# Kernel tuning notes

Hardware: AMD Instinct MI355X
Metric: run time of the kernel (lower is better)

The kernel has to match this reference:

```python
import jax, jax.numpy as jnp
import numpy as np

B, W, N, F_IN = 2, 8, 10000, 5
E = 80000
H = 128


def setup_inputs() -> dict:
    key = jax.random.key(0)
    ks = jax.random.split(key, 16)
    s = 0.05
    inp = {
        "x": jax.random.normal(ks[0], (B, W, N, F_IN), dtype=jnp.float32),
        "edge_index": jax.random.randint(ks[1], (2, E), 0, N, dtype=jnp.int64),
        # GCN layer 1 (in_features -> hidden) and layer 2 (hidden -> hidden)
        "gcn1_w": jax.random.normal(ks[2], (F_IN, H), dtype=jnp.float32) * s,
        "gcn1_b": jnp.zeros((H,), dtype=jnp.float32),
        "gcn2_w": jax.random.normal(ks[3], (H, H), dtype=jnp.float32) * s,
        "gcn2_b": jnp.zeros((H,), dtype=jnp.float32),
        # LSTM (torch gate order: i, f, g, o)
        "lstm_w_ih": jax.random.normal(ks[4], (4 * H, H), dtype=jnp.float32) * s,
        "lstm_w_hh": jax.random.normal(ks[5], (4 * H, H), dtype=jnp.float32) * s,
        "lstm_b_ih": jnp.zeros((4 * H,), dtype=jnp.float32),
        "lstm_b_hh": jnp.zeros((4 * H,), dtype=jnp.float32),
        # Decoder MLP: H -> H//2 -> 1
        "dec_w1": jax.random.normal(ks[6], (H, H // 2), dtype=jnp.float32) * s,
        "dec_b1": jnp.zeros((H // 2,), dtype=jnp.float32),
        "dec_w2": jax.random.normal(ks[7], (H // 2, 1), dtype=jnp.float32) * s,
        "dec_b2": jnp.zeros((1,), dtype=jnp.float32),
    }
    return inp


def _forward(x, edge_index, gcn1_w, gcn1_b, gcn2_w, gcn2_b,
             lstm_w_ih, lstm_w_hh, lstm_b_ih, lstm_b_hh,
             dec_w1, dec_b1, dec_w2, dec_b2):
    b, w, n, f_in = x.shape
    h_dim = gcn1_w.shape[1]
    # --- GCN normalization (PyG GCNConv default: add self-loops, sym-norm) ---
    loop = jnp.arange(n, dtype=edge_index.dtype)
    src = jnp.concatenate([edge_index[0], loop])
    dst = jnp.concatenate([edge_index[1], loop])
    deg = jnp.zeros((n,), x.dtype).at[dst].add(jnp.float32(1.0))
    dinv = jax.lax.rsqrt(deg)
    norm = dinv[src] * dinv[dst]  # (E+N,)

    def gcn(h, wm, bias):
        # h: (BW, N, Fin) -> (BW, N, H). Transform-then-aggregate (linear op).
        ht = h @ wm                                   # (BW, N, H)
        msg = ht[:, src, :] * norm[None, :, None]      # (BW, E+N, H)
        agg = jnp.zeros_like(ht).at[:, dst, :].add(msg)
        return agg + bias

    xf = x.reshape(b * w, n, f_in)
    h = jax.nn.relu(gcn(xf, gcn1_w, gcn1_b))   # dropout is identity at eval
    h = jax.nn.relu(gcn(h, gcn2_w, gcn2_b))

    # (BW, N, H) -> (B, N, W, H) -> (B*N, W, H): per-node temporal sequences
    h = h.reshape(b, w, n, h_dim).transpose(0, 2, 1, 3).reshape(b * n, w, h_dim)

    # --- single-layer LSTM, keep only last hidden state ---
    def step(carry, xt):
        hp, cp = carry
        gates = xt @ lstm_w_ih.T + hp @ lstm_w_hh.T + lstm_b_ih + lstm_b_hh
        i, f, g, o = jnp.split(gates, 4, axis=-1)
        c = jax.nn.sigmoid(f) * cp + jax.nn.sigmoid(i) * jnp.tanh(g)
        hn = jax.nn.sigmoid(o) * jnp.tanh(c)
        return (hn, c), None

    init = (jnp.zeros((b * n, h_dim), x.dtype), jnp.zeros((b * n, h_dim), x.dtype))
    (h_last, _), _ = jax.lax.scan(step, init, h.transpose(1, 0, 2))  # scan over W

    # --- MLP decoder ---
    d = jax.nn.relu(h_last @ dec_w1 + dec_b1)
    pred = (d @ dec_w2 + dec_b2)[..., 0]
    return pred.reshape(b, n)


def reference(x, edge_index, gcn1_w, gcn1_b, gcn2_w, gcn2_b,
              lstm_w_ih, lstm_w_hh, lstm_b_ih, lstm_b_hh,
              dec_w1, dec_b1, dec_w2, dec_b2):
    return _forward(x, edge_index, gcn1_w, gcn1_b, gcn2_w, gcn2_b,
                    lstm_w_ih, lstm_w_hh, lstm_b_ih, lstm_b_hh,
                    dec_w1, dec_b1, dec_w2, dec_b2)
```

## Files before the change

### kernel.cpp

```cpp
#include <hip/hip_runtime.h>
#include <hip/hip_fp16.h>
#include <cstdint>
#include <cstddef>

#define Bn   2
#define Wn   8
#define Nn   10000
#define Fin  5
#define En   80000
#define Hn   128
#define BWn  (Bn*Wn)
#define ROWS (BWn*Nn)
#define MR   (Bn*Nn)
#define LROWS 32

typedef _Float16 half8 __attribute__((ext_vector_type(8)));
typedef float f32x4 __attribute__((ext_vector_type(4)));

#define LOG2E 1.44269504088896f

__device__ __forceinline__ float fast_sigmoid(float x) {
    return __builtin_amdgcn_rcpf(1.f + __builtin_amdgcn_exp2f(-LOG2E * x));
}
__device__ __forceinline__ float fast_tanh(float x) {
    return fmaf(-2.f, __builtin_amdgcn_rcpf(1.f + __builtin_amdgcn_exp2f(2.f * LOG2E * x)), 1.f);
}

__global__ __launch_bounds__(256) void setup_kernel(
    const int* __restrict__ ei, const float* __restrict__ bih, const float* __restrict__ bhh,
    const float* __restrict__ wih, const float* __restrict__ whh,
    const float* __restrict__ g2w, const float* __restrict__ x,
    int* __restrict__ counts, float* __restrict__ bsum,
    _Float16* __restrict__ wif, _Float16* __restrict__ whf,
    _Float16* __restrict__ g2wt, float* __restrict__ xt) {
    __shared__ float buf[6400];
    const int b = blockIdx.x;
    const int tid = threadIdx.x;
    if (b < 313) {
        int e = b * 256 + tid;
        if (e < En) atomicAdd(&counts[ei[En + e]], 1);
    } else if (b < 315) {
        int i = (b - 313) * 256 + tid;
        if (i < 4 * Hn) bsum[i] = bih[i] + bhh[i];
    } else if (b < 891) {
        int i = (b - 315) * 256 + tid;
        if (i < 131072) {
            int idx = i & 65535;
            int j = idx & 7, lane = (idx >> 3) & 63, kt = (idx >> 9) & 3, ct = idx >> 11;
            int n = ct * 16 + (lane & 15);
            int k = kt * 32 + (lane >> 4) * 8 + j;
            if (i < 65536) wif[idx] = (_Float16)wih[n * 128 + k];
            else           whf[idx] = (_Float16)whh[n * 128 + k];
        } else {
            int j = i - 131072;
            int n = j >> 7, k = j & 127;
            g2wt[j] = (_Float16)g2w[k * Hn + n];
        }
    } else {
        const int n0 = (b - 891) * 80;
        for (int i = tid; i < 6400; i += 256) {
            int s = i / 400, r = i - s * 400;
            int node = r / 5, f = r - node * 5;
            buf[(node * 16 + s) * 5 + f] = x[((size_t)s * Nn + n0) * 5 + r];
        }
        __syncthreads();
        float* dst = xt + (size_t)n0 * 80;
        for (int i = tid; i < 6400; i += 256) dst[i] = buf[i];
    }
}

enum { CHUNK = 10 };
static_assert(CHUNK * 1024 >= Nn, "scan chunk");

__global__ __launch_bounds__(1024) void scan_kernel(
    const int* __restrict__ counts, int* __restrict__ row_ptr,
    int* __restrict__ fill_ptr, float* __restrict__ dinv) {
    __shared__ int sums[1024];
    const int t = threadIdx.x;
    const int base = t * CHUNK;
    int cnt[CHUNK];
    int s = 0;
    #pragma unroll
    for (int i = 0; i < CHUNK; ++i) {
        int idx = base + i;
        int v = (idx < Nn) ? counts[idx] + 1 : 0;
        cnt[i] = v; s += v;
    }
    sums[t] = s;
    __syncthreads();
    for (int off = 1; off < 1024; off <<= 1) {
        int v = (t >= off) ? sums[t - off] : 0;
        __syncthreads();
        sums[t] += v;
        __syncthreads();
    }
    int excl = (t == 0) ? 0 : sums[t - 1];
    #pragma unroll
    for (int i = 0; i < CHUNK; ++i) {
        int idx = base + i;
        if (idx < Nn) {
            row_ptr[idx] = excl;
            fill_ptr[idx] = excl;
            dinv[idx] = rsqrtf((float)cnt[i]);
            excl += cnt[i];
        }
    }
    if (t == 1023) row_ptr[Nn] = excl;
}

__global__ void fill_kernel(const int* __restrict__ ei,
                            const float* __restrict__ dinv,
                            int* fill_ptr, int* __restrict__ col,
                            float* __restrict__ wgt) {
    int i = blockIdx.x * blockDim.x + threadIdx.x;
    if (i < Nn) {
        int p = atomicAdd(&fill_ptr[i], 1);
        col[p] = i;
        wgt[p] = dinv[i] * dinv[i];
    } else if (i < Nn + En) {
        int e = i - Nn;
        int s = ei[e];
        int d = ei[En + e];
        int p = atomicAdd(&fill_ptr[d], 1);
        col[p] = s;
        wgt[p] = dinv[s] * dinv[d];
    }
}

__global__ __launch_bounds__(128) void agg_x_kernel(
    const float* __restrict__ xt, const int* __restrict__ row_ptr,
    const int* __restrict__ col, const float* __restrict__ wgt,
    float* __restrict__ aggx) {
    const int n = blockIdx.x;
    const int t = threadIdx.x;
    const int s = t >> 3, f = t & 7;
    if (f >= Fin) return;
    const int start = row_ptr[n], end = row_ptr[n + 1];
    const int off = s * 5 + f;
    float acc = 0.f;
    for (int e = start; e < end; ++e)
        acc = fmaf(wgt[e], xt[(size_t)col[e] * 80 + off], acc);
    aggx[(size_t)n * 80 + off] = acc;
}

__global__ __launch_bounds__(256) void gcn2_fused_kernel(
    const float* __restrict__ aggx, const float* __restrict__ w1,
    const float* __restrict__ b1, const _Float16* __restrict__ g2wt,
    _Float16* __restrict__ C) {
    __shared__ __align__(16) _Float16 s_buf[128][136];
    __shared__ _Float16 Bs[128][40];
    const int tid = threadIdx.x;
    const int m0 = blockIdx.x * 128;
    {
        const int rg = tid >> 4;
        const int cg = tid & 15;
        float wreg[Fin][8], breg[8];
        #pragma unroll
        for (int k = 0; k < 8; ++k) breg[k] = b1[cg * 8 + k];
        #pragma unroll
        for (int f = 0; f < Fin; ++f)
            #pragma unroll
            for (int k = 0; k < 8; ++k) wreg[f][k] = w1[f * Hn + cg * 8 + k];
        #pragma unroll
        for (int rr = 0; rr < 8; ++rr) {
            const float* ar = aggx + (size_t)(m0 + rg * 8 + rr) * Fin;
            float a[Fin];
            #pragma unroll
            for (int f = 0; f < Fin; ++f) a[f] = ar[f];
            half8 v;
            #pragma unroll
            for (int k = 0; k < 8; ++k) {
                float s = breg[k];
                #pragma unroll
                for (int f = 0; f < Fin; ++f) s = fmaf(a[f], wreg[f][k], s);
                v[k] = (_Float16)fmaxf(s, 0.f);
            }
            *(half8*)&s_buf[rg * 8 + rr][cg * 8] = v;
        }
    }
    __syncthreads();
    const int wave = tid >> 6, lane = tid & 63;
    const int l = lane & 15, q = lane >> 4;
    const int wm = (wave & 1) * 64, wn = (wave >> 1) * 64;
    f32x4 acc[4][4];
    #pragma unroll
    for (int i = 0; i < 4; ++i)
        #pragma unroll
        for (int j = 0; j < 4; ++j) acc[i][j] = (f32x4){0.f, 0.f, 0.f, 0.f};
    for (int kt = 0; kt < 128; kt += 32) {
        #pragma unroll
        for (int j = 0; j < 2; ++j) {
            int idx = tid + j * 256;
            int r = idx >> 2, c = (idx & 3) * 8;
            *(half8*)&Bs[r][c] = *(const half8*)(g2wt + (size_t)r * 128 + kt + c);
        }
        __syncthreads();
        half8 af[4], bf[4];
        #pragma unroll
        for (int i = 0; i < 4; ++i) af[i] = *(const half8*)&s_buf[wm + i * 16 + l][kt + q * 8];
        #pragma unroll
        for (int j = 0; j < 4; ++j) bf[j] = *(const half8*)&Bs[wn + j * 16 + l][q * 8];
        #pragma unroll
        for (int i = 0; i < 4; ++i)
            #pragma unroll
            for (int j = 0; j < 4; ++j)
                acc[i][j] = __builtin_amdgcn_mfma_f32_16x16x32_f16(
                    af[i], bf[j], acc[i][j], 0, 0, 0);
        __syncthreads();
    }
    #pragma unroll
    for (int j = 0; j < 4; ++j) {
        int ccol = wn + j * 16 + l;
        #pragma unroll
        for (int i = 0; i < 4; ++i)
            #pragma unroll
            for (int r = 0; r < 4; ++r)
                s_buf[wm + i * 16 + q * 4 + r][ccol] = (_Float16)acc[i][j][r];
    }
    __syncthreads();
    const size_t base = (size_t)m0 * 128;
    #pragma unroll
    for (int it = 0; it < 8; ++it) {
        int idx = it * 256 + tid;
        int row = idx >> 4, ch = (idx & 15) * 8;
        *(half8*)(C + base + (size_t)row * 128 + ch) = *(const half8*)&s_buf[row][ch];
    }
}

__global__ __launch_bounds__(256) void gcn_agg2_kernel(
    const _Float16* __restrict__ ht, const int* __restrict__ row_ptr,
    const int* __restrict__ col, const float* __restrict__ wgt,
    const float* __restrict__ bias, _Float16* __restrict__ out) {
    const int n = blockIdx.x;
    const int t = threadIdx.x;
    const int s = t >> 4;
    const int g = (t & 15) * 8;
    const int start = row_ptr[n], end = row_ptr[n + 1];
    float acc[8];
    #pragma unroll
    for (int j = 0; j < 8; ++j) acc[j] = 0.f;
    for (int e = start; e < end; ++e) {
        const int c = col[e];
        const float w = wgt[e];
        half8 v = *(const half8*)(ht + ((size_t)c * BWn + s) * Hn + g);
        #pragma unroll
        for (int j = 0; j < 8; ++j) acc[j] = fmaf(w, (float)v[j], acc[j]);
    }
    half8 o;
    #pragma unroll
    for (int j = 0; j < 8; ++j) o[j] = (_Float16)fmaxf(acc[j] + bias[g + j], 0.f);
    *(half8*)(out + ((size_t)n * BWn + s) * Hn + g) = o;
}

__global__ __launch_bounds__(512, 1) void lstm_fused3_kernel(
    const _Float16* __restrict__ h2, const _Float16* __restrict__ wif,
    const _Float16* __restrict__ whf, const float* __restrict__ bsum,
    const float* __restrict__ dw1, const float* __restrict__ db1,
    const float* __restrict__ dw2, const float* __restrict__ db2,
    float* __restrict__ out) {
    __shared__ __align__(16) _Float16 x_lds[2][LROWS][144];
    __shared__ __align__(16) _Float16 h_lds[2][LROWS][144];
    const int tid = threadIdx.x;
    const int nw = tid >> 6, lane = tid & 63;
    const int l = lane & 15, q = lane >> 4;
    const int r0 = blockIdx.x * LROWS;
    const int srow = tid >> 4, sch = (tid & 15) * 8;
    const int sgrow = r0 + srow;
    const int sb = (sgrow >= Nn) ? 1 : 0;
    const int sn = sgrow - sb * Nn;
    const _Float16* xbase = h2 + ((size_t)sn * BWn + sb * Wn) * 128 + sch;

    half8 wic[4][4], whc[4][4];
    #pragma unroll
    for (int g = 0; g < 4; ++g) {
        int ct = g * 8 + nw;
        #pragma unroll
        for (int kt = 0; kt < 4; ++kt) {
            wic[g][kt] = *(const half8*)(wif + (((size_t)ct * 4 + kt) * 64 + lane) * 8);
            whc[g][kt] = *(const half8*)(whf + (((size_t)ct * 4 + kt) * 64 + lane) * 8);
        }
    }
    float bias[4];
    #pragma unroll
    for (int g = 0; g < 4; ++g) bias[g] = bsum[g * 128 + nw * 16 + l];
    float c_reg[2][4];
    #pragma unroll
    for (int i = 0; i < 2; ++i)
        #pragma unroll
        for (int r = 0; r < 4; ++r) c_reg[i][r] = 0.f;

    *(half8*)&x_lds[0][srow][sch] = *(const half8*)(xbase);
    __syncthreads();

    for (int t = 0; t < Wn; ++t) {
        half8 xv = {0, 0, 0, 0, 0, 0, 0, 0};
        if (t + 1 < Wn) xv = *(const half8*)(xbase + (size_t)(t + 1) * 128);

        f32x4 acc[2][4];
        #pragma unroll
        for (int i = 0; i < 2; ++i)
            #pragma unroll
            for (int g = 0; g < 4; ++g)
                acc[i][g] = (f32x4){bias[g], bias[g], bias[g], bias[g]};

        #pragma unroll
        for (int kt = 0; kt < 4; ++kt) {
            half8 af[2];
            #pragma unroll
            for (int i = 0; i < 2; ++i)
                af[i] = *(const half8*)&x_lds[t & 1][i * 16 + l][kt * 32 + q * 8];
            #pragma unroll
            for (int i = 0; i < 2; ++i)
                #pragma unroll
                for (int g = 0; g < 4; ++g)
                    acc[i][g] = __builtin_amdgcn_mfma_f32_16x16x32_f16(
                        af[i], wic[g][kt], acc[i][g], 0, 0, 0);
        }
        if (t > 0) {
            #pragma unroll
            for (int kt = 0; kt < 4; ++kt) {
                half8 af[2];
                #pragma unroll
                for (int i = 0; i < 2; ++i)
                    af[i] = *(const half8*)&h_lds[t & 1][i * 16 + l][kt * 32 + q * 8];
                #pragma unroll
                for (int i = 0; i < 2; ++i)
                    #pragma unroll
                    for (int g = 0; g < 4; ++g)
                        acc[i][g] = __builtin_amdgcn_mfma_f32_16x16x32_f16(
                            af[i], whc[g][kt], acc[i][g], 0, 0, 0);
            }
        }
        #pragma unroll
        for (int i = 0; i < 2; ++i) {
            #pragma unroll
            for (int r = 0; r < 4; ++r) {
                float si = fast_sigmoid(acc[i][0][r]);
                float sf = fast_sigmoid(acc[i][1][r]);
                float tg = fast_tanh(acc[i][2][r]);
                float so = fast_sigmoid(acc[i][3][r]);
                float cn = sf * c_reg[i][r] + si * tg;
                c_reg[i][r] = cn;
                h_lds[(t + 1) & 1][i * 16 + q * 4 + r][nw * 16 + l] =
                    (_Float16)(so * fast_tanh(cn));
            }
        }
        if (t + 1 < Wn) *(half8*)&x_lds[(t + 1) & 1][srow][sch] = xv;
        __syncthreads();
    }

    #pragma unroll
    for (int rr = 0; rr < 4; ++rr) {
        const int row = nw + rr * 8;
        float d = db1[lane];
        #pragma unroll
        for (int k8 = 0; k8 < 16; ++k8) {
            half8 hv = *(const half8*)&h_lds[0][row][k8 * 8];
            #pragma unroll
            for (int j = 0; j < 8; ++j)
                d = fmaf((float)hv[j], dw1[(k8 * 8 + j) * 64 + lane], d);
        }
        d = fmaxf(d, 0.f);
        float p = d * dw2[lane];
        #pragma unroll
        for (int off = 32; off; off >>= 1) p += __shfl_down(p, off);
        if (lane == 0) out[r0 + row] = p + db2[0];
    }
}


extern "C" void kernel_launch(void* const* d_in, const int* in_sizes, int n_in,
                              void* d_out, int out_size, void* d_ws, size_t ws_size,
                              hipStream_t stream) {
    const float* x   = (const float*)d_in[0];
    const int*   ei  = (const int*)d_in[1];
    const float* g1w = (const float*)d_in[2];
    const float* g1b = (const float*)d_in[3];
    const float* g2w = (const float*)d_in[4];
    const float* g2b = (const float*)d_in[5];
    const float* wih = (const float*)d_in[6];
    const float* whh = (const float*)d_in[7];
    const float* bih = (const float*)d_in[8];
    const float* bhh = (const float*)d_in[9];
    const float* dw1 = (const float*)d_in[10];
    const float* db1 = (const float*)d_in[11];
    const float* dw2 = (const float*)d_in[12];
    const float* db2 = (const float*)d_in[13];
    float* out = (float*)d_out;

    char* p = (char*)d_ws;
    auto alloc = [&](size_t bytes) {
        char* r = p;
        p += (bytes + 255) & ~(size_t)255;
        return r;
    };
    int*      counts   = (int*)     alloc(Nn * 4);
    int*      row_ptr  = (int*)     alloc((Nn + 1) * 4);
    int*      fill_ptr = (int*)     alloc((Nn + 1) * 4);
    float*    dinv     = (float*)   alloc(Nn * 4);
    float*    bsum     = (float*)   alloc(4 * Hn * 4);
    int*      col      = (int*)     alloc((En + Nn) * 4);
    float*    wgt      = (float*)   alloc((En + Nn) * 4);
    _Float16* wif      = (_Float16*)alloc(512 * 128 * 2);
    _Float16* whf      = (_Float16*)alloc(512 * 128 * 2);
    _Float16* g2wt     = (_Float16*)alloc(128 * 128 * 2);
    float*    xt       = (float*)   alloc((size_t)Nn * 80 * 4);
    float*    aggx     = (float*)   alloc((size_t)ROWS * Fin * 4);
    _Float16* htf      = (_Float16*)alloc((size_t)ROWS * Hn * 2);
    _Float16* h2f      = (_Float16*)alloc((size_t)ROWS * Hn * 2);

    hipMemsetAsync(counts, 0, Nn * 4, stream);

    setup_kernel<<<1016, 256, 0, stream>>>(ei, bih, bhh, wih, whh, g2w, x,
                                           counts, bsum, wif, whf, g2wt, xt);
    scan_kernel<<<1, 1024, 0, stream>>>(counts, row_ptr, fill_ptr, dinv);
    fill_kernel<<<(Nn + En + 255) / 256, 256, 0, stream>>>(ei, dinv, fill_ptr, col, wgt);

    agg_x_kernel<<<Nn, 128, 0, stream>>>(xt, row_ptr, col, wgt, aggx);

    gcn2_fused_kernel<<<ROWS / 128, 256, 0, stream>>>(aggx, g1w, g1b, g2wt, htf);

    gcn_agg2_kernel<<<Nn, 256, 0, stream>>>(htf, row_ptr, col, wgt, g2b, h2f);

    lstm_fused3_kernel<<<MR / LROWS, 512, 0, stream>>>(
        h2f, wif, whf, bsum, dw1, db1, dw2, db2, out);
}
```

Baseline: 291.3 us.

## Split decoder out of LSTM kernel and single-buffer the hidden state

Moves the MLP decoder out of the fused LSTM kernel into its own launch. The LSTM now writes its final hidden states to a global fp16 buffer, which the decoder reads back. The hidden-state LDS buffer goes from double to single buffering, which needs an extra barrier per timestep before the hidden state is overwritten. This looks like an unfusion that trades an extra launch and a global round trip, plus more synchronisation, for lower LDS use and simpler LSTM code.

```diff
diff --git a/kernel.cpp b/kernel.cpp
--- a/kernel.cpp
+++ b/kernel.cpp
@@ -252,14 +252,12 @@
     *(half8*)(out + ((size_t)n * BWn + s) * Hn + g) = o;
 }
 
-__global__ __launch_bounds__(512, 1) void lstm_fused3_kernel(
+__global__ __launch_bounds__(512, 1) void lstm_fused2_kernel(
     const _Float16* __restrict__ h2, const _Float16* __restrict__ wif,
     const _Float16* __restrict__ whf, const float* __restrict__ bsum,
-    const float* __restrict__ dw1, const float* __restrict__ db1,
-    const float* __restrict__ dw2, const float* __restrict__ db2,
-    float* __restrict__ out) {
+    _Float16* __restrict__ hf) {
     __shared__ __align__(16) _Float16 x_lds[2][LROWS][144];
-    __shared__ __align__(16) _Float16 h_lds[2][LROWS][144];
+    __shared__ __align__(16) _Float16 h_lds[LROWS][144];
     const int tid = threadIdx.x;
     const int nw = tid >> 6, lane = tid & 63;
     const int l = lane & 15, q = lane >> 4;
@@ -322,7 +320,7 @@
                 half8 af[2];
                 #pragma unroll
                 for (int i = 0; i < 2; ++i)
-                    af[i] = *(const half8*)&h_lds[t & 1][i * 16 + l][kt * 32 + q * 8];
+                    af[i] = *(const half8*)&h_lds[i * 16 + l][kt * 32 + q * 8];
                 #pragma unroll
                 for (int i = 0; i < 2; ++i)
                     #pragma unroll
@@ -331,6 +329,8 @@
                             af[i], whc[g][kt], acc[i][g], 0, 0, 0);
             }
         }
+        __syncthreads();
+
         #pragma unroll
         for (int i = 0; i < 2; ++i) {
             #pragma unroll
@@ -341,31 +341,32 @@
                 float so = fast_sigmoid(acc[i][3][r]);
                 float cn = sf * c_reg[i][r] + si * tg;
                 c_reg[i][r] = cn;
-                h_lds[(t + 1) & 1][i * 16 + q * 4 + r][nw * 16 + l] =
-                    (_Float16)(so * fast_tanh(cn));
+                h_lds[i * 16 + q * 4 + r][nw * 16 + l] = (_Float16)(so * fast_tanh(cn));
             }
         }
         if (t + 1 < Wn) *(half8*)&x_lds[(t + 1) & 1][srow][sch] = xv;
         __syncthreads();
     }
-
-    #pragma unroll
-    for (int rr = 0; rr < 4; ++rr) {
-        const int row = nw + rr * 8;
-        float d = db1[lane];
-        #pragma unroll
-        for (int k8 = 0; k8 < 16; ++k8) {
-            half8 hv = *(const half8*)&h_lds[0][row][k8 * 8];
-            #pragma unroll
-            for (int j = 0; j < 8; ++j)
-                d = fmaf((float)hv[j], dw1[(k8 * 8 + j) * 64 + lane], d);
-        }
-        d = fmaxf(d, 0.f);
-        float p = d * dw2[lane];
-        #pragma unroll
-        for (int off = 32; off; off >>= 1) p += __shfl_down(p, off);
-        if (lane == 0) out[r0 + row] = p + db2[0];
-    }
+    *(half8*)(hf + (size_t)sgrow * 128 + sch) = *(const half8*)&h_lds[srow][sch];
+}
+
+__global__ __launch_bounds__(256) void decoder_kernel(
+    const _Float16* __restrict__ h, const float* __restrict__ w1,
+    const float* __restrict__ b1, const float* __restrict__ w2,
+    const float* __restrict__ b2, float* __restrict__ out) {
+    const int wave = threadIdx.x >> 6;
+    const int lane = threadIdx.x & 63;
+    const int row = blockIdx.x * 4 + wave;
+    if (row >= MR) return;
+    const _Float16* hr = h + (size_t)row * Hn;
+    float d = b1[lane];
+    #pragma unroll 8
+    for (int k = 0; k < Hn; ++k) d = fmaf((float)hr[k], w1[k * 64 + lane], d);
+    d = fmaxf(d, 0.f);
+    float p = d * w2[lane];
+    #pragma unroll
+    for (int off = 32; off; off >>= 1) p += __shfl_down(p, off);
+    if (lane == 0) out[row] = p + b2[0];
 }
 
 
@@ -408,6 +409,7 @@
     float*    aggx     = (float*)   alloc((size_t)ROWS * Fin * 4);
     _Float16* htf      = (_Float16*)alloc((size_t)ROWS * Hn * 2);
     _Float16* h2f      = (_Float16*)alloc((size_t)ROWS * Hn * 2);
+    _Float16* hf       = (_Float16*)alloc((size_t)MR * Hn * 2);
 
     hipMemsetAsync(counts, 0, Nn * 4, stream);
 
@@ -422,6 +424,7 @@
 
     gcn_agg2_kernel<<<Nn, 256, 0, stream>>>(htf, row_ptr, col, wgt, g2b, h2f);
 
-    lstm_fused3_kernel<<<MR / LROWS, 512, 0, stream>>>(
-        h2f, wif, whf, bsum, dw1, db1, dw2, db2, out);
-}
+    lstm_fused2_kernel<<<MR / LROWS, 512, 0, stream>>>(h2f, wif, whf, bsum, hf);
+
+    decoder_kernel<<<(MR + 3) / 4, 256, 0, stream>>>(hf, dw1, db1, dw2, db2, out);
+}
```

Measured after the change: 282.5 us. 3.0% less time.
